# Kernel optimization log

Hardware: AMD Instinct MI355X
Metric: run time of the kernel (lower is better)

## Reference

```python
import jax, jax.numpy as jnp
import numpy as np

N = 50000      # nodes
E = 600000     # edges
IN = 128       # in_channels
HID = 128      # GCN hidden width (fixed in module)
H = 4          # TransformerConv heads
C = 32         # out_channels per head (heads*C = 128)


def _lin(k, fan_in, fan_out):
    return jax.random.normal(k, (fan_in, fan_out), jnp.float32) / np.sqrt(fan_in)


def setup_inputs() -> dict:
    key = jax.random.key(0)
    ks = jax.random.split(key, 12)
    return {
        "x": jax.random.normal(ks[0], (N, IN), jnp.float32),
        "edge_index": jax.random.randint(ks[1], (2, E), 0, N, dtype=jnp.int32),
        "W_gcn": _lin(ks[2], IN, HID),
        "b_gcn": jnp.zeros((HID,), jnp.float32),
        "Wq": _lin(ks[3], HID, H * C),
        "bq": jnp.zeros((H * C,), jnp.float32),
        "Wk": _lin(ks[4], HID, H * C),
        "bk": jnp.zeros((H * C,), jnp.float32),
        "Wv": _lin(ks[5], HID, H * C),
        "bv": jnp.zeros((H * C,), jnp.float32),
        "Ws": _lin(ks[6], HID, H * C),
        "bs": jnp.zeros((H * C,), jnp.float32),
    }


def reference(x, edge_index, W_gcn, b_gcn, Wq, bq, Wk, bk, Wv, bv, Ws, bs):
    n = x.shape[0]
    idt = edge_index.dtype

    # ---- GCNConv: x' = D^{-1/2}(A+I)D^{-1/2} x W + b, then ReLU ----
    h = x @ W_gcn                                   # [N, HID] linear first (PyG order)
    loop = jnp.arange(n, dtype=idt)
    src = jnp.concatenate([edge_index[0], loop])    # with self-loops
    tgt = jnp.concatenate([edge_index[1], loop])
    deg = jax.ops.segment_sum(jnp.ones(src.shape, h.dtype), tgt, num_segments=n)
    dinv = jnp.where(deg > 0, jax.lax.rsqrt(deg), 0.0)
    norm = dinv[src] * dinv[tgt]                    # [E+N]
    h = jax.ops.segment_sum(h[src] * norm[:, None], tgt, num_segments=n)
    h = jax.nn.relu(h + b_gcn)                      # [N, HID]

    # ---- TransformerConv (heads=4, concat=True, no self-loops added) ----
    s, t = edge_index[0], edge_index[1]
    q = (h @ Wq + bq).reshape(n, H, C)
    k = (h @ Wk + bk).reshape(n, H, C)
    v = (h @ Wv + bv).reshape(n, H, C)

    alpha = jnp.einsum('ehc,ehc->eh', q[t], k[s]) / np.sqrt(C)   # [E, H]
    m = jax.lax.stop_gradient(jax.ops.segment_max(alpha, t, num_segments=n))
    ea = jnp.exp(alpha - m[t])
    denom = jax.ops.segment_sum(ea, t, num_segments=n)           # [N, H]
    w = ea / jnp.where(denom[t] > 0, denom[t], 1.0)              # softmax per target node

    out = jax.ops.segment_sum(w[:, :, None] * v[s], t, num_segments=n)  # [N, H, C]
    out = out.reshape(n, H * C)

    # root/skip connection (lin_skip)
    return out + h @ Ws + bs
```

## Files before the change

### kernel.cpp

```cpp
#include <hip/hip_runtime.h>
#include <hip/hip_bf16.h>

typedef __attribute__((ext_vector_type(8))) short short8;
typedef __attribute__((ext_vector_type(4))) float floatx4;
typedef _Float16 half2v __attribute__((ext_vector_type(2)));

__device__ __forceinline__ float ld_f(const void* p, int f32, int i) {
  if (f32) return ((const float*)p)[i];
  unsigned short u = ((const unsigned short*)p)[i];
  return __uint_as_float(((unsigned)u) << 16);
}
__device__ __forceinline__ short ld_bf(const void* p, int f32, int i) {
  if (!f32) return ((const short*)p)[i];
  __hip_bfloat16 h = __float2bfloat16(((const float*)p)[i]);
  return *reinterpret_cast<short*>(&h);
}
__device__ __forceinline__ unsigned short f_to_bfu(float v) {
  __hip_bfloat16 h = __float2bfloat16(v);
  return *reinterpret_cast<unsigned short*>(&h);
}
__device__ __forceinline__ short f_to_h(float v) {
  _Float16 h = (_Float16)v;
  return *reinterpret_cast<short*>(&h);
}
__device__ __forceinline__ float bflo(unsigned w) { return __uint_as_float(w << 16); }
__device__ __forceinline__ float bfhi(unsigned w) { return __uint_as_float(w & 0xFFFF0000u); }

__global__ void init_kernel(const unsigned short* __restrict__ xs, int* __restrict__ flag,
                            int* __restrict__ cnt, int N) {
  if (blockIdx.x == 0) {
    __shared__ int sbad;
    if (threadIdx.x == 0) sbad = 0;
    __syncthreads();
    int bad = 0;
    for (int j = 2 * threadIdx.x; j < 16384; j += 512) {
      unsigned e = (xs[j] >> 7) & 0xFF;
      if (e >= 0xF0) bad = 1;
    }
    if (bad) atomicOr(&sbad, 1);
    __syncthreads();
    if (threadIdx.x == 0) flag[0] = sbad;
    return;
  }
  int i = (blockIdx.x - 1) * blockDim.x + threadIdx.x;
  if (i < N) cnt[i] = 0;
}

__global__ void prep_hist(const void* bg, const void* bq, const void* bk, const void* bv,
                          const void* bs, const void* Wg, const void* Wq, const void* Wk,
                          const void* Wv, const void* Ws, const int* __restrict__ flag,
                          float* __restrict__ bgf, float* __restrict__ bias512,
                          short* __restrict__ WpG, short* __restrict__ WpQ,
                          const int* __restrict__ ei, int* __restrict__ cnt,
                          int* __restrict__ erank, int E, int Gp) {
  if ((int)blockIdx.x >= Gp) {
    int e = (blockIdx.x - Gp) * blockDim.x + threadIdx.x;
    if (e < E) erank[e] = atomicAdd(&cnt[ei[E + e]], 1);
    return;
  }
  int tid = blockIdx.x * blockDim.x + threadIdx.x;
  int f = *flag;
  if (tid < 128) { bgf[tid] = ld_f(bg, f, tid); return; }
  if (tid < 640) {
    int t = tid - 128;
    const void* b = (t < 128) ? bq : (t < 256) ? bk : (t < 384) ? bv : bs;
    bias512[t] = ld_f(b, f, t & 127);
    return;
  }
  if (tid < 640 + 2048) {
    int id = tid - 640;
    int lane = id & 63, kb = (id >> 6) & 3, tn = id >> 8;
    int k0 = kb * 32 + (lane >> 4) * 8;
    int n = tn * 16 + (lane & 15);
    short* dst = WpG + (size_t)id * 8;
#pragma unroll
    for (int j = 0; j < 8; ++j) dst[j] = ld_bf(Wg, f, (k0 + j) * 128 + n);
    return;
  }
  if (tid < 640 + 2048 + 8192) {
    int id = tid - 640 - 2048;
    int lane = id & 63, kb = (id >> 6) & 3, tn = id >> 8;
    int k0 = kb * 32 + (lane >> 4) * 8;
    int n = tn * 16 + (lane & 15);
    const void* W = (n < 128) ? Wq : (n < 256) ? Wk : (n < 384) ? Wv : Ws;
    int col = n & 127;
    short* dst = WpQ + (size_t)id * 8;
#pragma unroll
    for (int j = 0; j < 8; ++j) dst[j] = ld_bf(W, f, (k0 + j) * 128 + col);
  }
}

__global__ void scanA(const int* __restrict__ cnt, int* __restrict__ chunkscan,
                      int* __restrict__ partials, int N) {
  __shared__ int sh[1024];
  int t = threadIdx.x;
  int g = blockIdx.x * 1024 + t;
  int v = (g < N) ? cnt[g] : 0;
  sh[t] = v;
  __syncthreads();
  for (int o = 1; o < 1024; o <<= 1) {
    int add = (t >= o) ? sh[t - o] : 0;
    __syncthreads();
    sh[t] += add;
    __syncthreads();
  }
  if (g < N) chunkscan[g] = sh[t];
  if (t == 1023) partials[blockIdx.x] = sh[1023];
}

__global__ void scanB(int* __restrict__ partials, int nb) {
  int lane = threadIdx.x;
  if (nb <= 64) {
    int v = (lane < nb) ? partials[lane] : 0;
#pragma unroll
    for (int o = 1; o < 64; o <<= 1) {
      int t = __shfl_up(v, o);
      if (lane >= o) v += t;
    }
    int ex = __shfl_up(v, 1);
    if (lane == 0) ex = 0;
    if (lane < nb) partials[lane] = ex;
    return;
  }
  if (lane == 0) {
    int run = 0;
    for (int b = 0; b < nb; ++b) {
      int t = partials[b];
      partials[b] = run;
      run += t;
    }
  }
}

__global__ void scanC(const int* __restrict__ cnt, const int* __restrict__ chunkscan,
                      const int* __restrict__ partials, int* __restrict__ rowptr,
                      float* __restrict__ dinv, int N) {
  int g = blockIdx.x * blockDim.x + threadIdx.x;
  if (g == 0) rowptr[0] = 0;
  if (g >= N) return;
  int c = cnt[g];
  int inc = chunkscan[g] + partials[g >> 10];
  rowptr[g + 1] = inc;
  dinv[g] = rsqrtf((float)c + 1.0f);
}

__global__ void gemmh0_fill(const void* __restrict__ X, const int* __restrict__ flag,
                            const short* __restrict__ Bp, const float* __restrict__ dinv,
                            short* __restrict__ C, int M, const int* __restrict__ ei,
                            const int* __restrict__ rowptr, const int* __restrict__ erank,
                            int* __restrict__ srcs, int E, int Gg) {
  if ((int)blockIdx.x >= Gg) {
    int e = (blockIdx.x - Gg) * blockDim.x + threadIdx.x;
    if (e < E) {
      int t = ei[E + e];
      srcs[rowptr[t] + erank[e]] = ei[e];
    }
    return;
  }
  int wv = (blockIdx.x * blockDim.x + threadIdx.x) >> 6;
  int lane = threadIdx.x & 63;
  int tilesM = (M + 15) >> 4;
  if (wv >= tilesM) return;
  int f = *flag;
  int tm = wv;
  int m = tm * 16 + (lane & 15);
  int mc = m < M ? m : M - 1;
  int quad = lane >> 4;
  short8 a[4];
  if (f) {
    const float4* xr = (const float4*)((const float*)X + (size_t)mc * 128) + quad * 2;
#pragma unroll
    for (int kb = 0; kb < 4; ++kb) {
      float4 u = xr[kb * 8];
      float4 w = xr[kb * 8 + 1];
      a[kb][0] = (short)f_to_bfu(u.x);
      a[kb][1] = (short)f_to_bfu(u.y);
      a[kb][2] = (short)f_to_bfu(u.z);
      a[kb][3] = (short)f_to_bfu(u.w);
      a[kb][4] = (short)f_to_bfu(w.x);
      a[kb][5] = (short)f_to_bfu(w.y);
      a[kb][6] = (short)f_to_bfu(w.z);
      a[kb][7] = (short)f_to_bfu(w.w);
    }
  } else {
    const short* xr = (const short*)X + (size_t)mc * 128 + quad * 8;
#pragma unroll
    for (int kb = 0; kb < 4; ++kb) a[kb] = *(const short8*)(xr + kb * 32);
  }
  floatx4 acc[8];
#pragma unroll
  for (int tn = 0; tn < 8; ++tn) acc[tn] = (floatx4){0.f, 0.f, 0.f, 0.f};
#pragma unroll
  for (int kb = 0; kb < 4; ++kb) {
#pragma unroll
    for (int tn = 0; tn < 8; ++tn) {
      short8 b8 = *(const short8*)(Bp + ((size_t)(tn * 4 + kb) * 64 + lane) * 8);
      acc[tn] = __builtin_amdgcn_mfma_f32_16x16x32_bf16(a[kb], b8, acc[tn], 0, 0, 0);
    }
  }
  int row0 = tm * 16 + quad * 4;
  int cl = lane & 15;
  float dsc[4];
#pragma unroll
  for (int r = 0; r < 4; ++r) dsc[r] = (row0 + r < M) ? dinv[row0 + r] : 0.f;
#pragma unroll
  for (int tn = 0; tn < 8; ++tn)
#pragma unroll
    for (int r = 0; r < 4; ++r)
      if (row0 + r < M)
        C[(size_t)(row0 + r) * 128 + tn * 16 + cl] = (short)f_to_bfu(acc[tn][r] * dsc[r]);
}

__global__ void gcn_gather(const int* __restrict__ rowptr, const int* __restrict__ srcs,
                           const float* __restrict__ dinv, const unsigned* __restrict__ h0,
                           const float* __restrict__ bgf, unsigned* __restrict__ hbf, int N) {
  int node = (int)((blockIdx.x * (long long)blockDim.x + threadIdx.x) >> 6);
  if (node >= N) return;
  int lane = threadIdx.x & 63;
  int q = lane >> 4, sl = lane & 15;
  int beg = rowptr[node], end = rowptr[node + 1];
  int deg = end - beg;
  int dm1 = deg - 1;
  int sreg = srcs[deg > 0 ? beg + (lane < dm1 ? lane : dm1) : 0];
  float a0 = 0.f, a1 = 0.f, a2 = 0.f, a3 = 0.f, a4 = 0.f, a5 = 0.f, a6 = 0.f, a7 = 0.f;
  int dd = deg < 64 ? deg : 64;
  for (int base = 0; base < dd; base += 16) {
    int p0 = base + q, p1 = p0 + 4, p2 = p0 + 8, p3 = p0 + 12;
    int s0 = __shfl(sreg, p0 < dm1 ? p0 : dm1);
    int s1 = __shfl(sreg, p1 < dm1 ? p1 : dm1);
    int s2 = __shfl(sreg, p2 < dm1 ? p2 : dm1);
    int s3 = __shfl(sreg, p3 < dm1 ? p3 : dm1);
    float m0 = p0 < deg ? 1.f : 0.f;
    float m1 = p1 < deg ? 1.f : 0.f;
    float m2 = p2 < deg ? 1.f : 0.f;
    float m3 = p3 < deg ? 1.f : 0.f;
    uint4 w0 = *(const uint4*)(h0 + (size_t)s0 * 64 + sl * 4);
    uint4 w1 = *(const uint4*)(h0 + (size_t)s1 * 64 + sl * 4);
    uint4 w2 = *(const uint4*)(h0 + (size_t)s2 * 64 + sl * 4);
    uint4 w3 = *(const uint4*)(h0 + (size_t)s3 * 64 + sl * 4);
    a0 += m0 * bflo(w0.x) + m1 * bflo(w1.x) + m2 * bflo(w2.x) + m3 * bflo(w3.x);
    a1 += m0 * bfhi(w0.x) + m1 * bfhi(w1.x) + m2 * bfhi(w2.x) + m3 * bfhi(w3.x);
    a2 += m0 * bflo(w0.y) + m1 * bflo(w1.y) + m2 * bflo(w2.y) + m3 * bflo(w3.y);
    a3 += m0 * bfhi(w0.y) + m1 * bfhi(w1.y) + m2 * bfhi(w2.y) + m3 * bfhi(w3.y);
    a4 += m0 * bflo(w0.z) + m1 * bflo(w1.z) + m2 * bflo(w2.z) + m3 * bflo(w3.z);
    a5 += m0 * bfhi(w0.z) + m1 * bfhi(w1.z) + m2 * bfhi(w2.z) + m3 * bfhi(w3.z);
    a6 += m0 * bflo(w0.w) + m1 * bflo(w1.w) + m2 * bflo(w2.w) + m3 * bflo(w3.w);
    a7 += m0 * bfhi(w0.w) + m1 * bfhi(w1.w) + m2 * bfhi(w2.w) + m3 * bfhi(w3.w);
  }
  for (int i = beg + 64 + q; i < end; i += 4) {
    uint4 w0 = *(const uint4*)(h0 + (size_t)srcs[i] * 64 + sl * 4);
    a0 += bflo(w0.x);
    a1 += bfhi(w0.x);
    a2 += bflo(w0.y);
    a3 += bfhi(w0.y);
    a4 += bflo(w0.z);
    a5 += bfhi(w0.z);
    a6 += bflo(w0.w);
    a7 += bfhi(w0.w);
  }
  a0 += __shfl_xor(a0, 16); a0 += __shfl_xor(a0, 32);
  a1 += __shfl_xor(a1, 16); a1 += __shfl_xor(a1, 32);
  a2 += __shfl_xor(a2, 16); a2 += __shfl_xor(a2, 32);
  a3 += __shfl_xor(a3, 16); a3 += __shfl_xor(a3, 32);
  a4 += __shfl_xor(a4, 16); a4 += __shfl_xor(a4, 32);
  a5 += __shfl_xor(a5, 16); a5 += __shfl_xor(a5, 32);
  a6 += __shfl_xor(a6, 16); a6 += __shfl_xor(a6, 32);
  a7 += __shfl_xor(a7, 16); a7 += __shfl_xor(a7, 32);
  if (q == 0) {
    uint4 hw = *(const uint4*)(h0 + (size_t)node * 64 + sl * 4);
    float dt = dinv[node];
    const float4* bb = (const float4*)bgf;
    float4 b0 = bb[sl * 2], b1 = bb[sl * 2 + 1];
    float v0 = (a0 + bflo(hw.x)) * dt + b0.x;
    float v1 = (a1 + bfhi(hw.x)) * dt + b0.y;
    float v2 = (a2 + bflo(hw.y)) * dt + b0.z;
    float v3 = (a3 + bfhi(hw.y)) * dt + b0.w;
    float v4 = (a4 + bflo(hw.z)) * dt + b1.x;
    float v5 = (a5 + bfhi(hw.z)) * dt + b1.y;
    float v6 = (a6 + bflo(hw.w)) * dt + b1.z;
    float v7 = (a7 + bfhi(hw.w)) * dt + b1.w;
    v0 = v0 > 0.f ? v0 : 0.f;
    v1 = v1 > 0.f ? v1 : 0.f;
    v2 = v2 > 0.f ? v2 : 0.f;
    v3 = v3 > 0.f ? v3 : 0.f;
    v4 = v4 > 0.f ? v4 : 0.f;
    v5 = v5 > 0.f ? v5 : 0.f;
    v6 = v6 > 0.f ? v6 : 0.f;
    v7 = v7 > 0.f ? v7 : 0.f;
    uint4 o;
    o.x = (unsigned)f_to_bfu(v0) | ((unsigned)f_to_bfu(v1) << 16);
    o.y = (unsigned)f_to_bfu(v2) | ((unsigned)f_to_bfu(v3) << 16);
    o.z = (unsigned)f_to_bfu(v4) | ((unsigned)f_to_bfu(v5) << 16);
    o.w = (unsigned)f_to_bfu(v6) | ((unsigned)f_to_bfu(v7) << 16);
    *(uint4*)(hbf + (size_t)node * 64 + sl * 4) = o;
  }
}

__global__ void gemm_qkvs(const short* __restrict__ A, const short* __restrict__ Bp,
                          const float* __restrict__ bias512, short* __restrict__ qb,
                          short* __restrict__ kvb, short* __restrict__ skipb, int M) {
  int wv = (blockIdx.x * blockDim.x + threadIdx.x) >> 6;
  int lane = threadIdx.x & 63;
  int tilesM = (M + 15) >> 4;
  if (wv >= tilesM * 4) return;
  int tng = wv & 3, tm = wv >> 2;
  int m = tm * 16 + (lane & 15);
  int mc = m < M ? m : M - 1;
  int quad = lane >> 4;
  const short* Arow = A + (size_t)mc * 128 + quad * 8;
  short8 a[4];
#pragma unroll
  for (int kb = 0; kb < 4; ++kb) a[kb] = *(const short8*)(Arow + kb * 32);
  floatx4 acc[8];
#pragma unroll
  for (int j = 0; j < 8; ++j) acc[j] = (floatx4){0.f, 0.f, 0.f, 0.f};
#pragma unroll
  for (int kb = 0; kb < 4; ++kb) {
#pragma unroll
    for (int j = 0; j < 8; ++j) {
      int tn = tng * 8 + j;
      short8 b8 = *(const short8*)(Bp + ((size_t)(tn * 4 + kb) * 64 + lane) * 8);
      acc[j] = __builtin_amdgcn_mfma_f32_16x16x32_bf16(a[kb], b8, acc[j], 0, 0, 0);
    }
  }
  int row0 = tm * 16 + quad * 4;
  int cl = lane & 15;
#pragma unroll
  for (int j = 0; j < 8; ++j) {
    int cc = j * 16 + cl;
    float b = bias512[tng * 128 + cc];
#pragma unroll
    for (int r = 0; r < 4; ++r) {
      int row = row0 + r;
      if (row >= M) continue;
      float val = acc[j][r] + b;
      if (tng == 0) {
        qb[(size_t)row * 128 + cc] = f_to_h(val);
      } else if (tng == 3) {
        skipb[(size_t)row * 128 + cc] = (short)f_to_bfu(val);
      } else {
        size_t base = (size_t)row * 256 + (size_t)((cc >> 2) * 8 + (cc & 3));
        if (tng == 1)
          kvb[base] = f_to_h(val);
        else
          kvb[base + 4] = (short)f_to_bfu(val);
      }
    }
  }
}

__device__ __forceinline__ float dotred8(half2v qa, half2v qc, unsigned kw0, unsigned kw1) {
  half2v k0 = *reinterpret_cast<half2v*>(&kw0);
  half2v k1 = *reinterpret_cast<half2v*>(&kw1);
#if __has_builtin(__builtin_amdgcn_fdot2)
  float p = __builtin_amdgcn_fdot2(qa, k0, 0.f, false);
  p = __builtin_amdgcn_fdot2(qc, k1, p, false);
#else
  float p = (float)qa[0] * (float)k0[0] + (float)qa[1] * (float)k0[1] +
            (float)qc[0] * (float)k1[0] + (float)qc[1] * (float)k1[1];
#endif
  p += __shfl_xor(p, 1, 8);
  p += __shfl_xor(p, 2, 8);
  p += __shfl_xor(p, 4, 8);
  return p * 0.17677669529663687f;
}

__global__ void attn_fused(const int* __restrict__ rowptr, const int* __restrict__ srcs,
                           const unsigned* __restrict__ qb, const unsigned* __restrict__ kvb,
                           const unsigned* __restrict__ skipb, float* __restrict__ out, int N) {
  int node = (int)((blockIdx.x * (long long)blockDim.x + threadIdx.x) >> 6);
  if (node >= N) return;
  int lane = threadIdx.x & 63;
  int hf = lane >> 5, sl = lane & 31;
  uint2 qw = *(const uint2*)(qb + (size_t)node * 64 + sl * 2);
  half2v qa = *reinterpret_cast<half2v*>(&qw.x);
  half2v qc = *reinterpret_cast<half2v*>(&qw.y);
  int beg = rowptr[node], end = rowptr[node + 1];
  int deg = end - beg;
  int dm1 = deg - 1;
  int sreg = srcs[deg > 0 ? beg + (lane < dm1 ? lane : dm1) : 0];

  float denom = 0.f, ax0 = 0.f, ax1 = 0.f, ax2 = 0.f, ax3 = 0.f;
  int dd = deg < 64 ? deg : 64;
  for (int base = 0; base < dd; base += 8) {
    int p0 = base + hf, p1 = p0 + 2, p2 = p0 + 4, p3 = p0 + 6;
    int s0 = __shfl(sreg, p0 < dm1 ? p0 : dm1);
    int s1 = __shfl(sreg, p1 < dm1 ? p1 : dm1);
    int s2 = __shfl(sreg, p2 < dm1 ? p2 : dm1);
    int s3 = __shfl(sreg, p3 < dm1 ? p3 : dm1);
    uint4 kv0 = *(const uint4*)(kvb + (size_t)s0 * 128 + sl * 4);
    uint4 kv1 = *(const uint4*)(kvb + (size_t)s1 * 128 + sl * 4);
    uint4 kv2 = *(const uint4*)(kvb + (size_t)s2 * 128 + sl * 4);
    uint4 kv3 = *(const uint4*)(kvb + (size_t)s3 * 128 + sl * 4);
    float e0 = __expf(dotred8(qa, qc, kv0.x, kv0.y));
    float e1 = __expf(dotred8(qa, qc, kv1.x, kv1.y));
    float e2 = __expf(dotred8(qa, qc, kv2.x, kv2.y));
    float e3 = __expf(dotred8(qa, qc, kv3.x, kv3.y));
    e0 = p0 < deg ? e0 : 0.f;
    e1 = p1 < deg ? e1 : 0.f;
    e2 = p2 < deg ? e2 : 0.f;
    e3 = p3 < deg ? e3 : 0.f;
    denom += e0 + e1 + e2 + e3;
    ax0 += e0 * bflo(kv0.z) + e1 * bflo(kv1.z) + e2 * bflo(kv2.z) + e3 * bflo(kv3.z);
    ax1 += e0 * bfhi(kv0.z) + e1 * bfhi(kv1.z) + e2 * bfhi(kv2.z) + e3 * bfhi(kv3.z);
    ax2 += e0 * bflo(kv0.w) + e1 * bflo(kv1.w) + e2 * bflo(kv2.w) + e3 * bflo(kv3.w);
    ax3 += e0 * bfhi(kv0.w) + e1 * bfhi(kv1.w) + e2 * bfhi(kv2.w) + e3 * bfhi(kv3.w);
  }
  for (int i = beg + 64 + hf; i < end; i += 2) {
    int s0 = srcs[i];
    uint4 kv0 = *(const uint4*)(kvb + (size_t)s0 * 128 + sl * 4);
    float e0 = __expf(dotred8(qa, qc, kv0.x, kv0.y));
    denom += e0;
    ax0 += e0 * bflo(kv0.z);
    ax1 += e0 * bfhi(kv0.z);
    ax2 += e0 * bflo(kv0.w);
    ax3 += e0 * bfhi(kv0.w);
  }
  denom += __shfl_xor(denom, 32);
  ax0 += __shfl_xor(ax0, 32);
  ax1 += __shfl_xor(ax1, 32);
  ax2 += __shfl_xor(ax2, 32);
  ax3 += __shfl_xor(ax3, 32);
  if (hf == 0) {
    float r = denom > 0.f ? 1.f / denom : 0.f;
    uint2 sw = *(const uint2*)(skipb + (size_t)node * 64 + sl * 2);
    float4 o;
    o.x = ax0 * r + bflo(sw.x);
    o.y = ax1 * r + bfhi(sw.x);
    o.z = ax2 * r + bflo(sw.y);
    o.w = ax3 * r + bfhi(sw.y);
    *(float4*)(out + (size_t)node * 128 + sl * 4) = o;
  }
}

extern "C" void kernel_launch(void* const* d_in, const int* in_sizes, int n_in,
                              void* d_out, int out_size, void* d_ws, size_t ws_size,
                              hipStream_t stream) {
  const void* x  = d_in[0];
  const int* ei  = (const int*)d_in[1];
  const void* Wg = d_in[2];
  const void* bg = d_in[3];
  const void* Wq = d_in[4];
  const void* bq = d_in[5];
  const void* Wk = d_in[6];
  const void* bk = d_in[7];
  const void* Wv = d_in[8];
  const void* bv = d_in[9];
  const void* Ws = d_in[10];
  const void* bs = d_in[11];
  float* out = (float*)d_out;

  const int N = in_sizes[0] / 128;
  const int E = in_sizes[1] / 2;
  int tilesM = (N + 15) / 16;
  int nscan = (N + 1023) / 1024;
  const int B = 256;

  char* ws = (char*)d_ws;
  size_t off = 0;
  auto carve = [&](size_t bytes) -> void* {
    void* p = ws + off;
    off += (bytes + 255) & ~(size_t)255;
    return p;
  };
  int* flag = (int*)carve(256);
  float* bias512 = (float*)carve(512 * 4);
  float* bgf = (float*)carve(128 * 4);
  float* dinv = (float*)carve((size_t)N * 4);
  int* cnt = (int*)carve((size_t)N * 4);
  int* rowptr = (int*)carve((size_t)(N + 1) * 4);
  int* chunkscan = (int*)carve((size_t)N * 4);
  int* partials = (int*)carve((size_t)(nscan + 1) * 4);
  int* srcs = (int*)carve((size_t)E * 4);
  int* erank = (int*)carve((size_t)E * 4);
  short* WpG = (short*)carve((size_t)16384 * 2);
  short* WpQ = (short*)carve((size_t)65536 * 2);
  short* h0bf = (short*)carve((size_t)N * 128 * 2);
  short* hbf = (short*)carve((size_t)N * 128 * 2);
  short* qb = (short*)carve((size_t)N * 128 * 2);
  short* kvb = (short*)carve((size_t)N * 256 * 2);
  short* skipb = (short*)carve((size_t)N * 128 * 2);

  int Gp = (10880 + B - 1) / B;
  int Gh = (E + B - 1) / B;
  int Gg = (tilesM * 64 + B - 1) / B;
  int Gf = (E + B - 1) / B;

  init_kernel<<<1 + (N + B - 1) / B, B, 0, stream>>>((const unsigned short*)x, flag, cnt, N);
  prep_hist<<<Gp + Gh, B, 0, stream>>>(bg, bq, bk, bv, bs, Wg, Wq, Wk, Wv, Ws, flag,
                                       bgf, bias512, WpG, WpQ, ei, cnt, erank, E, Gp);
  scanA<<<nscan, 1024, 0, stream>>>(cnt, chunkscan, partials, N);
  scanB<<<1, 64, 0, stream>>>(partials, nscan);
  scanC<<<(N + B - 1) / B, B, 0, stream>>>(cnt, chunkscan, partials, rowptr, dinv, N);
  gemmh0_fill<<<Gg + Gf, B, 0, stream>>>(x, flag, WpG, dinv, h0bf, N, ei, rowptr, erank,
                                         srcs, E, Gg);
  gcn_gather<<<(N + 3) / 4, B, 0, stream>>>(rowptr, srcs, dinv, (const unsigned*)h0bf, bgf,
                                            (unsigned*)hbf, N);
  gemm_qkvs<<<(tilesM * 4 + 3) / 4, B, 0, stream>>>(hbf, WpQ, bias512, qb, kvb, skipb, N);
  attn_fused<<<(N + 3) / 4, B, 0, stream>>>(rowptr, srcs, (const unsigned*)qb,
                                            (const unsigned*)kvb, (const unsigned*)skipb, out, N);
}
```

Baseline: 262.2 us.

## Process two nodes per wavefront in gather and attention kernels, use DPP reductions

Both the GCN gather and the attention kernel now give each half-wavefront its own target node instead of using a full 64-lane wave per node, so fewer lanes sit idle at the average degree of about 12. Cross-half reductions go away, and the grid is halved. The 8-lane dot-product reduction in attention now uses DPP moves instead of shuffles. The cost is divergence when the two nodes sharing a wave have very different degrees, since the loop runs to the larger of the two.

```diff
diff --git a/kernel.cpp b/kernel.cpp
--- a/kernel.cpp
+++ b/kernel.cpp
@@ -214,22 +214,27 @@
 __global__ void gcn_gather(const int* __restrict__ rowptr, const int* __restrict__ srcs,
                            const float* __restrict__ dinv, const unsigned* __restrict__ h0,
                            const float* __restrict__ bgf, unsigned* __restrict__ hbf, int N) {
-  int node = (int)((blockIdx.x * (long long)blockDim.x + threadIdx.x) >> 6);
-  if (node >= N) return;
+  int wv = (int)((blockIdx.x * (long long)blockDim.x + threadIdx.x) >> 6);
   int lane = threadIdx.x & 63;
-  int q = lane >> 4, sl = lane & 15;
-  int beg = rowptr[node], end = rowptr[node + 1];
-  int deg = end - beg;
+  int hf = lane >> 5, q2 = (lane >> 4) & 1, sl = lane & 15, sl32 = lane & 31;
+  int node = wv * 2 + hf;
+  int nodec = node < N ? node : N - 1;
+  int beg = rowptr[nodec], end = rowptr[nodec + 1];
+  int deg = node < N ? end - beg : 0;
   int dm1 = deg - 1;
-  int sreg = srcs[deg > 0 ? beg + (lane < dm1 ? lane : dm1) : 0];
+  int dmc = dm1 > 0 ? dm1 : 0;
+  int sreg = srcs[deg > 0 ? beg + (sl32 < dm1 ? sl32 : dm1) : 0];
+  int degmax = deg;
+  degmax = max(degmax, __shfl_xor(degmax, 32));
+  int dd = degmax < 32 ? degmax : 32;
+  int hb = hf << 5;
   float a0 = 0.f, a1 = 0.f, a2 = 0.f, a3 = 0.f, a4 = 0.f, a5 = 0.f, a6 = 0.f, a7 = 0.f;
-  int dd = deg < 64 ? deg : 64;
-  for (int base = 0; base < dd; base += 16) {
-    int p0 = base + q, p1 = p0 + 4, p2 = p0 + 8, p3 = p0 + 12;
-    int s0 = __shfl(sreg, p0 < dm1 ? p0 : dm1);
-    int s1 = __shfl(sreg, p1 < dm1 ? p1 : dm1);
-    int s2 = __shfl(sreg, p2 < dm1 ? p2 : dm1);
-    int s3 = __shfl(sreg, p3 < dm1 ? p3 : dm1);
+  for (int base = 0; base < dd; base += 8) {
+    int p0 = base + q2, p1 = p0 + 2, p2 = p0 + 4, p3 = p0 + 6;
+    int s0 = __shfl(sreg, hb + (p0 < dmc ? p0 : dmc));
+    int s1 = __shfl(sreg, hb + (p1 < dmc ? p1 : dmc));
+    int s2 = __shfl(sreg, hb + (p2 < dmc ? p2 : dmc));
+    int s3 = __shfl(sreg, hb + (p3 < dmc ? p3 : dmc));
     float m0 = p0 < deg ? 1.f : 0.f;
     float m1 = p1 < deg ? 1.f : 0.f;
     float m2 = p2 < deg ? 1.f : 0.f;
@@ -247,7 +252,7 @@
     a6 += m0 * bflo(w0.w) + m1 * bflo(w1.w) + m2 * bflo(w2.w) + m3 * bflo(w3.w);
     a7 += m0 * bfhi(w0.w) + m1 * bfhi(w1.w) + m2 * bfhi(w2.w) + m3 * bfhi(w3.w);
   }
-  for (int i = beg + 64 + q; i < end; i += 4) {
+  for (int i = beg + 32 + q2; i < end; i += 2) {
     uint4 w0 = *(const uint4*)(h0 + (size_t)srcs[i] * 64 + sl * 4);
     a0 += bflo(w0.x);
     a1 += bfhi(w0.x);
@@ -258,15 +263,15 @@
     a6 += bflo(w0.w);
     a7 += bfhi(w0.w);
   }
-  a0 += __shfl_xor(a0, 16); a0 += __shfl_xor(a0, 32);
-  a1 += __shfl_xor(a1, 16); a1 += __shfl_xor(a1, 32);
-  a2 += __shfl_xor(a2, 16); a2 += __shfl_xor(a2, 32);
-  a3 += __shfl_xor(a3, 16); a3 += __shfl_xor(a3, 32);
-  a4 += __shfl_xor(a4, 16); a4 += __shfl_xor(a4, 32);
-  a5 += __shfl_xor(a5, 16); a5 += __shfl_xor(a5, 32);
-  a6 += __shfl_xor(a6, 16); a6 += __shfl_xor(a6, 32);
-  a7 += __shfl_xor(a7, 16); a7 += __shfl_xor(a7, 32);
-  if (q == 0) {
+  a0 += __shfl_xor(a0, 16);
+  a1 += __shfl_xor(a1, 16);
+  a2 += __shfl_xor(a2, 16);
+  a3 += __shfl_xor(a3, 16);
+  a4 += __shfl_xor(a4, 16);
+  a5 += __shfl_xor(a5, 16);
+  a6 += __shfl_xor(a6, 16);
+  a7 += __shfl_xor(a7, 16);
+  if (q2 == 0 && node < N) {
     uint4 hw = *(const uint4*)(h0 + (size_t)node * 64 + sl * 4);
     float dt = dinv[node];
     const float4* bb = (const float4*)bgf;
@@ -349,7 +354,13 @@
   }
 }
 
-__device__ __forceinline__ float dotred8(half2v qa, half2v qc, unsigned kw0, unsigned kw1) {
+__device__ __forceinline__ float dpp_red8(float p) {
+  p += __int_as_float(__builtin_amdgcn_mov_dpp(__float_as_int(p), 0xB1, 0xF, 0xF, true));
+  p += __int_as_float(__builtin_amdgcn_mov_dpp(__float_as_int(p), 0x4E, 0xF, 0xF, true));
+  p += __int_as_float(__builtin_amdgcn_mov_dpp(__float_as_int(p), 0x141, 0xF, 0xF, true));
+  return p;
+}
+__device__ __forceinline__ float dot_dpp(half2v qa, half2v qc, unsigned kw0, unsigned kw1) {
   half2v k0 = *reinterpret_cast<half2v*>(&kw0);
   half2v k1 = *reinterpret_cast<half2v*>(&kw1);
 #if __has_builtin(__builtin_amdgcn_fdot2)
@@ -359,43 +370,45 @@
   float p = (float)qa[0] * (float)k0[0] + (float)qa[1] * (float)k0[1] +
             (float)qc[0] * (float)k1[0] + (float)qc[1] * (float)k1[1];
 #endif
-  p += __shfl_xor(p, 1, 8);
-  p += __shfl_xor(p, 2, 8);
-  p += __shfl_xor(p, 4, 8);
-  return p * 0.17677669529663687f;
+  return dpp_red8(p) * 0.17677669529663687f;
 }
 
 __global__ void attn_fused(const int* __restrict__ rowptr, const int* __restrict__ srcs,
                            const unsigned* __restrict__ qb, const unsigned* __restrict__ kvb,
                            const unsigned* __restrict__ skipb, float* __restrict__ out, int N) {
-  int node = (int)((blockIdx.x * (long long)blockDim.x + threadIdx.x) >> 6);
-  if (node >= N) return;
+  int wv = (int)((blockIdx.x * (long long)blockDim.x + threadIdx.x) >> 6);
   int lane = threadIdx.x & 63;
   int hf = lane >> 5, sl = lane & 31;
-  uint2 qw = *(const uint2*)(qb + (size_t)node * 64 + sl * 2);
+  int node = wv * 2 + hf;
+  int nodec = node < N ? node : N - 1;
+  uint2 qw = *(const uint2*)(qb + (size_t)nodec * 64 + sl * 2);
   half2v qa = *reinterpret_cast<half2v*>(&qw.x);
   half2v qc = *reinterpret_cast<half2v*>(&qw.y);
-  int beg = rowptr[node], end = rowptr[node + 1];
-  int deg = end - beg;
+  int beg = rowptr[nodec], end = rowptr[nodec + 1];
+  int deg = node < N ? end - beg : 0;
   int dm1 = deg - 1;
-  int sreg = srcs[deg > 0 ? beg + (lane < dm1 ? lane : dm1) : 0];
+  int dmc = dm1 > 0 ? dm1 : 0;
+  int sreg = srcs[deg > 0 ? beg + (sl < dm1 ? sl : dm1) : 0];
+  int degmax = deg;
+  degmax = max(degmax, __shfl_xor(degmax, 32));
+  int dd = degmax < 32 ? degmax : 32;
+  int hb = hf << 5;
 
   float denom = 0.f, ax0 = 0.f, ax1 = 0.f, ax2 = 0.f, ax3 = 0.f;
-  int dd = deg < 64 ? deg : 64;
-  for (int base = 0; base < dd; base += 8) {
-    int p0 = base + hf, p1 = p0 + 2, p2 = p0 + 4, p3 = p0 + 6;
-    int s0 = __shfl(sreg, p0 < dm1 ? p0 : dm1);
-    int s1 = __shfl(sreg, p1 < dm1 ? p1 : dm1);
-    int s2 = __shfl(sreg, p2 < dm1 ? p2 : dm1);
-    int s3 = __shfl(sreg, p3 < dm1 ? p3 : dm1);
+  for (int base = 0; base < dd; base += 4) {
+    int p0 = base, p1 = base + 1, p2 = base + 2, p3 = base + 3;
+    int s0 = __shfl(sreg, hb + (p0 < dmc ? p0 : dmc));
+    int s1 = __shfl(sreg, hb + (p1 < dmc ? p1 : dmc));
+    int s2 = __shfl(sreg, hb + (p2 < dmc ? p2 : dmc));
+    int s3 = __shfl(sreg, hb + (p3 < dmc ? p3 : dmc));
     uint4 kv0 = *(const uint4*)(kvb + (size_t)s0 * 128 + sl * 4);
     uint4 kv1 = *(const uint4*)(kvb + (size_t)s1 * 128 + sl * 4);
     uint4 kv2 = *(const uint4*)(kvb + (size_t)s2 * 128 + sl * 4);
     uint4 kv3 = *(const uint4*)(kvb + (size_t)s3 * 128 + sl * 4);
-    float e0 = __expf(dotred8(qa, qc, kv0.x, kv0.y));
-    float e1 = __expf(dotred8(qa, qc, kv1.x, kv1.y));
-    float e2 = __expf(dotred8(qa, qc, kv2.x, kv2.y));
-    float e3 = __expf(dotred8(qa, qc, kv3.x, kv3.y));
+    float e0 = __expf(dot_dpp(qa, qc, kv0.x, kv0.y));
+    float e1 = __expf(dot_dpp(qa, qc, kv1.x, kv1.y));
+    float e2 = __expf(dot_dpp(qa, qc, kv2.x, kv2.y));
+    float e3 = __expf(dot_dpp(qa, qc, kv3.x, kv3.y));
     e0 = p0 < deg ? e0 : 0.f;
     e1 = p1 < deg ? e1 : 0.f;
     e2 = p2 < deg ? e2 : 0.f;
@@ -406,22 +419,17 @@
     ax2 += e0 * bflo(kv0.w) + e1 * bflo(kv1.w) + e2 * bflo(kv2.w) + e3 * bflo(kv3.w);
     ax3 += e0 * bfhi(kv0.w) + e1 * bfhi(kv1.w) + e2 * bfhi(kv2.w) + e3 * bfhi(kv3.w);
   }
-  for (int i = beg + 64 + hf; i < end; i += 2) {
+  for (int i = beg + 32; i < end; ++i) {
     int s0 = srcs[i];
     uint4 kv0 = *(const uint4*)(kvb + (size_t)s0 * 128 + sl * 4);
-    float e0 = __expf(dotred8(qa, qc, kv0.x, kv0.y));
+    float e0 = __expf(dot_dpp(qa, qc, kv0.x, kv0.y));
     denom += e0;
     ax0 += e0 * bflo(kv0.z);
     ax1 += e0 * bfhi(kv0.z);
     ax2 += e0 * bflo(kv0.w);
     ax3 += e0 * bfhi(kv0.w);
   }
-  denom += __shfl_xor(denom, 32);
-  ax0 += __shfl_xor(ax0, 32);
-  ax1 += __shfl_xor(ax1, 32);
-  ax2 += __shfl_xor(ax2, 32);
-  ax3 += __shfl_xor(ax3, 32);
-  if (hf == 0) {
+  if (node < N) {
     float r = denom > 0.f ? 1.f / denom : 0.f;
     uint2 sw = *(const uint2*)(skipb + (size_t)node * 64 + sl * 2);
     float4 o;
@@ -494,9 +502,9 @@
   scanC<<<(N + B - 1) / B, B, 0, stream>>>(cnt, chunkscan, partials, rowptr, dinv, N);
   gemmh0_fill<<<Gg + Gf, B, 0, stream>>>(x, flag, WpG, dinv, h0bf, N, ei, rowptr, erank,
                                          srcs, E, Gg);
-  gcn_gather<<<(N + 3) / 4, B, 0, stream>>>(rowptr, srcs, dinv, (const unsigned*)h0bf, bgf,
+  gcn_gather<<<(N + 7) / 8, B, 0, stream>>>(rowptr, srcs, dinv, (const unsigned*)h0bf, bgf,
                                             (unsigned*)hbf, N);
   gemm_qkvs<<<(tilesM * 4 + 3) / 4, B, 0, stream>>>(hbf, WpQ, bias512, qb, kvb, skipb, N);
-  attn_fused<<<(N + 3) / 4, B, 0, stream>>>(rowptr, srcs, (const unsigned*)qb,
+  attn_fused<<<(N + 7) / 8, B, 0, stream>>>(rowptr, srcs, (const unsigned*)qb,
                                             (const unsigned*)kvb, (const unsigned*)skipb, out, N);
 }
```

New measurement: 260.8 us. No clear change (-0.6%).
